# Optimization experiments

Hardware: AMD Instinct MI355X
Metric: run time of the kernel (lower is better)

The kernel has to match this reference:

```python
import jax, jax.numpy as jnp
import numpy as np

B, N_ATOMS = 8192, 64      # molecules, atoms per molecule
DIM, EXTRA, N_CLS = 70, 7, 11
N_FP = 10000               # fingerprint vocab


def setup_inputs() -> dict:
    key = jax.random.key(0)
    ks = jax.random.split(key, 9)
    atoms = jax.random.randint(ks[0], (B, N_ATOMS), 0, N_FP, dtype=jnp.int64 if jax.config.jax_enable_x64 else jnp.int32)
    adjacency = jax.random.uniform(ks[1], (B, N_ATOMS, N_ATOMS), dtype=jnp.float32)
    sel_desc = jax.random.normal(ks[2], (B, EXTRA), dtype=jnp.float32)
    embed_table = jax.random.normal(ks[3], (N_FP, DIM), dtype=jnp.float32)
    w1 = jax.random.normal(ks[4], (DIM, DIM), dtype=jnp.float32) * 0.05
    b1 = jax.random.normal(ks[5], (DIM,), dtype=jnp.float32) * 0.05
    w2 = jax.random.normal(ks[6], (DIM, DIM), dtype=jnp.float32) * 0.05
    b2 = jax.random.normal(ks[7], (DIM,), dtype=jnp.float32) * 0.05
    wp = jax.random.normal(ks[8], (DIM + EXTRA, N_CLS), dtype=jnp.float32) * 0.05
    bp = jnp.zeros((N_CLS,), dtype=jnp.float32)
    return {"atoms": atoms, "adjacency": adjacency, "sel_desc": sel_desc,
            "embed_table": embed_table, "w1": w1, "b1": b1,
            "w2": w2, "b2": b2, "wp": wp, "bp": bp}


def reference(atoms, adjacency, sel_desc, embed_table, w1, b1, w2, b2, wp, bp):
    # embed atoms: [B, n, dim]
    x = embed_table[atoms]
    # message-passing layers: relu(linear) then (block-diagonal == batched) adjacency matmul
    for w, b in ((w1, b1), (w2, b2)):
        h = jax.nn.relu(jnp.einsum('bnd,de->bne', x, w) + b)
        x = jnp.einsum('bnm,bmd->bnd', adjacency, h)
    # segment-sum pool over atoms per molecule (sum_axis)
    y = jnp.sum(x, axis=1)                       # [B, dim]
    y = jnp.concatenate([y, sel_desc], axis=1)   # [B, dim+extra]
    return jnp.einsum('bd,dc->bc', y, wp) + bp   # [B, 11]
```

## Files before the change

kernel.cpp:

```cpp
#include <hip/hip_runtime.h>
#include <hip/hip_bf16.h>

#define NFP    10000
#define DIM    70
#define GPAD   72
#define NATOMS 64
#define PGROWS 16

typedef short  short8  __attribute__((ext_vector_type(8)));
typedef float  floatx4 __attribute__((ext_vector_type(4)));

__device__ inline unsigned short f2bf(float f) {
  union { float f; unsigned u; } x; x.f = f;
  unsigned r = x.u + 0x7fffu + ((x.u >> 16) & 1u);
  return (unsigned short)(r >> 16);
}

__device__ inline ushort2 pk2bf(float a, float b) {
  __hip_bfloat162 h = __float22bfloat162_rn(make_float2(a, b));
  union { __hip_bfloat162 h; ushort2 u; } c; c.h = h; return c.u;
}

__global__ __launch_bounds__(256) void precompute_G(
    const float* __restrict__ emb, const float* __restrict__ w1,
    const float* __restrict__ b1,  const float* __restrict__ w2,
    unsigned short* __restrict__ G) {
  __shared__ float w1s[DIM * GPAD];
  __shared__ float w2s[DIM * GPAD];
  __shared__ float b1s[GPAD];
  __shared__ float embs[PGROWS * GPAD];
  __shared__ float e1s[PGROWS * GPAD];
  const int t = threadIdx.x;

  for (int i = t; i < DIM * GPAD; i += 256) {
    int r = i / GPAD, c = i % GPAD;
    float v1 = 0.f, v2 = 0.f;
    if (c < DIM) { v1 = w1[r * DIM + c]; v2 = w2[r * DIM + c]; }
    w1s[i] = v1; w2s[i] = v2;
  }
  if (t < GPAD) b1s[t] = (t < DIM) ? b1[t] : 0.f;
  const int row0 = blockIdx.x * PGROWS;
  for (int i = t; i < PGROWS * GPAD; i += 256) {
    int r = i / GPAD, c = i % GPAD;
    int vr = row0 + r;
    embs[i] = (vr < NFP && c < DIM) ? emb[vr * DIM + c] : 0.f;
  }
  __syncthreads();

  for (int task = t; task < PGROWS * 18; task += 256) {
    int r = task / 18, c4 = (task % 18) * 4;
    float4 acc = *(const float4*)&b1s[c4];
    for (int k = 0; k < DIM; k++) {
      float e = embs[r * GPAD + k];
      float4 w = *(const float4*)&w1s[k * GPAD + c4];
      acc.x = fmaf(e, w.x, acc.x); acc.y = fmaf(e, w.y, acc.y);
      acc.z = fmaf(e, w.z, acc.z); acc.w = fmaf(e, w.w, acc.w);
    }
    acc.x = fmaxf(acc.x, 0.f); acc.y = fmaxf(acc.y, 0.f);
    acc.z = fmaxf(acc.z, 0.f); acc.w = fmaxf(acc.w, 0.f);
    *(float4*)&e1s[r * GPAD + c4] = acc;
  }
  __syncthreads();

  for (int task = t; task < PGROWS * 18; task += 256) {
    int r = task / 18, c4 = (task % 18) * 4;
    int vr = row0 + r;
    if (vr >= NFP) continue;
    float ax = 0.f, ay = 0.f, az = 0.f, aw = 0.f;
    for (int k = 0; k < DIM; k++) {
      float e = e1s[r * GPAD + k];
      float4 w = *(const float4*)&w2s[k * GPAD + c4];
      ax = fmaf(e, w.x, ax); ay = fmaf(e, w.y, ay);
      az = fmaf(e, w.z, az); aw = fmaf(e, w.w, aw);
    }
    unsigned short* gp = G + vr * GPAD + c4;
    gp[0] = f2bf(ax); gp[1] = f2bf(ay); gp[2] = f2bf(az); gp[3] = f2bf(aw);
  }
}

__global__ __launch_bounds__(256) void mol_fused(
    const int* __restrict__ atoms, const float* __restrict__ adj,
    const float* __restrict__ sel, const float* __restrict__ b2,
    const float* __restrict__ wp,  const float* __restrict__ bp,
    const unsigned short* __restrict__ G, float* __restrict__ out) {
  __shared__ unsigned short adjs[64 * GPAD];
  __shared__ unsigned short gTs[80 * GPAD];
  __shared__ float cwave[4 * 64];
  __shared__ float b2p[80];
  __shared__ float yacc[4 * 80];
  __shared__ float yv[80];
  __shared__ int   satoms[64];

  const int b = blockIdx.x;
  const int t = threadIdx.x;
  const int w = t >> 6, lane = t & 63;
  const int q = lane >> 4, li = lane & 15;
  const int R = w * 16;

  if (t < 64) satoms[t] = atoms[b * 64 + t];
  if (t < 80) b2p[t] = (t < DIM) ? b2[t] : 0.f;
  __syncthreads();

  {
    const float* ap = adj + (size_t)b * 4096;
    const int mc = (t & 15) * 4;
    const int a  = t >> 4;
    float4 cs = make_float4(0.f, 0.f, 0.f, 0.f);
#pragma unroll
    for (int it = 0; it < 4; it++) {
      int n = a + 16 * it;
      float4 v = *(const float4*)(ap + n * 64 + mc);
      cs.x += v.x; cs.y += v.y; cs.z += v.z; cs.w += v.w;
      ushort2 lo = pk2bf(v.x, v.y);
      ushort2 hi = pk2bf(v.z, v.w);
      ushort4 u; u.x = lo.x; u.y = lo.y; u.z = hi.x; u.w = hi.y;
      *(ushort4*)&adjs[n * GPAD + mc] = u;
    }
#pragma unroll
    for (int s = 16; s <= 32; s <<= 1) {
      cs.x += __shfl_xor(cs.x, s); cs.y += __shfl_xor(cs.y, s);
      cs.z += __shfl_xor(cs.z, s); cs.w += __shfl_xor(cs.w, s);
    }
    if (((t >> 4) & 3) == 0) *(float4*)&cwave[w * 64 + mc] = cs;
  }

  {
    const int m = t & 63;
    const int row = satoms[m];
    const uint4* Gv = (const uint4*)G;
    for (int ch = w; ch < 9; ch += 4) {
      uint4 v = Gv[(unsigned)row * 9 + ch];
      unsigned short* gp = &gTs[(ch * 8) * GPAD + m];
      gp[0 * GPAD] = (unsigned short)(v.x & 0xffff);
      gp[1 * GPAD] = (unsigned short)(v.x >> 16);
      gp[2 * GPAD] = (unsigned short)(v.y & 0xffff);
      gp[3 * GPAD] = (unsigned short)(v.y >> 16);
      gp[4 * GPAD] = (unsigned short)(v.z & 0xffff);
      gp[5 * GPAD] = (unsigned short)(v.z >> 16);
      gp[6 * GPAD] = (unsigned short)(v.w & 0xffff);
      gp[7 * GPAD] = (unsigned short)(v.w >> 16);
    }
  }
  if (t < 72) {
    uint4 zz; zz.x = zz.y = zz.z = zz.w = 0u;
    *(uint4*)&gTs[72 * GPAD + t * 8] = zz;
  }
  __syncthreads();

  float cr[4];
#pragma unroll
  for (int r = 0; r < 4; r++) {
    int m = R + q * 4 + r;
    cr[r] = cwave[m] + cwave[64 + m] + cwave[128 + m] + cwave[192 + m];
  }

  short8 a0 = *(const short8*)&adjs[(R + li) * GPAD + q * 8];
  short8 a1 = *(const short8*)&adjs[(R + li) * GPAD + 32 + q * 8];
  floatx4 acc[5];
#pragma unroll
  for (int nt = 0; nt < 5; nt++) {
    floatx4 z = {0.f, 0.f, 0.f, 0.f};
    short8 b0 = *(const short8*)&gTs[(nt * 16 + li) * GPAD + q * 8];
    short8 b1 = *(const short8*)&gTs[(nt * 16 + li) * GPAD + 32 + q * 8];
    z = __builtin_amdgcn_mfma_f32_16x16x32_bf16(a0, b0, z, 0, 0, 0);
    z = __builtin_amdgcn_mfma_f32_16x16x32_bf16(a1, b1, z, 0, 0, 0);
    acc[nt] = z;
  }

  float ps[5];
#pragma unroll
  for (int nt = 0; nt < 5; nt++) {
    float bb = b2p[nt * 16 + li];
    float p = 0.f;
#pragma unroll
    for (int r = 0; r < 4; r++)
      p = fmaf(cr[r], fmaxf(acc[nt][r] + bb, 0.f), p);
    p += __shfl_xor(p, 16);
    p += __shfl_xor(p, 32);
    ps[nt] = p;
  }
  if (q == 0) {
#pragma unroll
    for (int nt = 0; nt < 5; nt++) yacc[w * 80 + nt * 16 + li] = ps[nt];
  }
  __syncthreads();

  if (t < 77) {
    float s;
    if (t < DIM) s = yacc[t] + yacc[80 + t] + yacc[160 + t] + yacc[240 + t];
    else         s = sel[(size_t)b * 7 + (t - DIM)];
    yv[t] = s;
  }
  __syncthreads();

  if (t < 11) {
    float s = bp[t];
#pragma unroll 11
    for (int d = 0; d < 77; d++) s = fmaf(yv[d], wp[d * 11 + t], s);
    out[(size_t)b * 11 + t] = s;
  }
}

extern "C" void kernel_launch(void* const* d_in, const int* in_sizes, int n_in,
                              void* d_out, int out_size, void* d_ws, size_t ws_size,
                              hipStream_t stream) {
  const int*   atoms = (const int*)d_in[0];
  const float* adj   = (const float*)d_in[1];
  const float* sel   = (const float*)d_in[2];
  const float* emb   = (const float*)d_in[3];
  const float* w1    = (const float*)d_in[4];
  const float* b1    = (const float*)d_in[5];
  const float* w2    = (const float*)d_in[6];
  const float* b2    = (const float*)d_in[7];
  const float* wp    = (const float*)d_in[8];
  const float* bp    = (const float*)d_in[9];

  const int B = in_sizes[0] / NATOMS;
  unsigned short* G = (unsigned short*)d_ws;

  precompute_G<<<(NFP + PGROWS - 1) / PGROWS, 256, 0, stream>>>(emb, w1, b1, w2, G);
  mol_fused<<<B, 256, 0, stream>>>(atoms, adj, sel, b2, wp, bp, G, (float*)d_out);
}
```

Measured before the change: 243.9 us.

## Hoist global loads, drop syncs, and parallelize final projection with wave shuffles

```diff
diff --git a/kernel.cpp b/kernel.cpp
--- a/kernel.cpp
+++ b/kernel.cpp
@@ -78,7 +78,7 @@
   }
 }
 
-__global__ __launch_bounds__(256) void mol_fused(
+__global__ __launch_bounds__(256, 7) void mol_fused(
     const int* __restrict__ atoms, const float* __restrict__ adj,
     const float* __restrict__ sel, const float* __restrict__ b2,
     const float* __restrict__ wp,  const float* __restrict__ bp,
@@ -86,72 +86,97 @@
   __shared__ unsigned short adjs[64 * GPAD];
   __shared__ unsigned short gTs[80 * GPAD];
   __shared__ float cwave[4 * 64];
-  __shared__ float b2p[80];
   __shared__ float yacc[4 * 80];
-  __shared__ float yv[80];
-  __shared__ int   satoms[64];
 
   const int b = blockIdx.x;
   const int t = threadIdx.x;
   const int w = t >> 6, lane = t & 63;
   const int q = lane >> 4, li = lane & 15;
   const int R = w * 16;
-
-  if (t < 64) satoms[t] = atoms[b * 64 + t];
-  if (t < 80) b2p[t] = (t < DIM) ? b2[t] : 0.f;
-  __syncthreads();
+  const int m = lane;
+
+  const int myAtom = atoms[b * 64 + m];
+  const float* ap = adj + (size_t)b * 4096;
+  const int mc = (t & 15) * 4;
+  const int a  = t >> 4;
+  float4 v0 = *(const float4*)(ap + (a     ) * 64 + mc);
+  float4 v1 = *(const float4*)(ap + (a + 16) * 64 + mc);
+  float4 v2 = *(const float4*)(ap + (a + 32) * 64 + mc);
+  float4 v3 = *(const float4*)(ap + (a + 48) * 64 + mc);
+  const uint4* Gv = (const uint4*)G;
+  uint4 g0 = Gv[(unsigned)myAtom * 9 + w];
+  uint4 g1 = Gv[(unsigned)myAtom * 9 + w + 4];
+  uint4 g2;
+  if (w == 0) g2 = Gv[(unsigned)myAtom * 9 + 8];
 
   {
-    const float* ap = adj + (size_t)b * 4096;
-    const int mc = (t & 15) * 4;
-    const int a  = t >> 4;
-    float4 cs = make_float4(0.f, 0.f, 0.f, 0.f);
-#pragma unroll
-    for (int it = 0; it < 4; it++) {
-      int n = a + 16 * it;
-      float4 v = *(const float4*)(ap + n * 64 + mc);
-      cs.x += v.x; cs.y += v.y; cs.z += v.z; cs.w += v.w;
-      ushort2 lo = pk2bf(v.x, v.y);
-      ushort2 hi = pk2bf(v.z, v.w);
-      ushort4 u; u.x = lo.x; u.y = lo.y; u.z = hi.x; u.w = hi.y;
-      *(ushort4*)&adjs[n * GPAD + mc] = u;
-    }
+    float4 cs;
+    cs.x = (v0.x + v1.x) + (v2.x + v3.x);
+    cs.y = (v0.y + v1.y) + (v2.y + v3.y);
+    cs.z = (v0.z + v1.z) + (v2.z + v3.z);
+    cs.w = (v0.w + v1.w) + (v2.w + v3.w);
 #pragma unroll
     for (int s = 16; s <= 32; s <<= 1) {
       cs.x += __shfl_xor(cs.x, s); cs.y += __shfl_xor(cs.y, s);
       cs.z += __shfl_xor(cs.z, s); cs.w += __shfl_xor(cs.w, s);
     }
     if (((t >> 4) & 3) == 0) *(float4*)&cwave[w * 64 + mc] = cs;
+
+    float4 vv[4] = {v0, v1, v2, v3};
+#pragma unroll
+    for (int it = 0; it < 4; it++) {
+      int n = a + 16 * it;
+      ushort2 lo = pk2bf(vv[it].x, vv[it].y);
+      ushort2 hi = pk2bf(vv[it].z, vv[it].w);
+      ushort4 u; u.x = lo.x; u.y = lo.y; u.z = hi.x; u.w = hi.y;
+      *(ushort4*)&adjs[n * GPAD + mc] = u;
+    }
   }
 
   {
-    const int m = t & 63;
-    const int row = satoms[m];
-    const uint4* Gv = (const uint4*)G;
-    for (int ch = w; ch < 9; ch += 4) {
-      uint4 v = Gv[(unsigned)row * 9 + ch];
-      unsigned short* gp = &gTs[(ch * 8) * GPAD + m];
-      gp[0 * GPAD] = (unsigned short)(v.x & 0xffff);
-      gp[1 * GPAD] = (unsigned short)(v.x >> 16);
-      gp[2 * GPAD] = (unsigned short)(v.y & 0xffff);
-      gp[3 * GPAD] = (unsigned short)(v.y >> 16);
-      gp[4 * GPAD] = (unsigned short)(v.z & 0xffff);
-      gp[5 * GPAD] = (unsigned short)(v.z >> 16);
-      gp[6 * GPAD] = (unsigned short)(v.w & 0xffff);
-      gp[7 * GPAD] = (unsigned short)(v.w >> 16);
-    }
-  }
-  if (t < 72) {
-    uint4 zz; zz.x = zz.y = zz.z = zz.w = 0u;
-    *(uint4*)&gTs[72 * GPAD + t * 8] = zz;
+    unsigned short* gp0 = &gTs[(w * 8) * GPAD + m];
+    gp0[0 * GPAD] = (unsigned short)(g0.x & 0xffff);
+    gp0[1 * GPAD] = (unsigned short)(g0.x >> 16);
+    gp0[2 * GPAD] = (unsigned short)(g0.y & 0xffff);
+    gp0[3 * GPAD] = (unsigned short)(g0.y >> 16);
+    gp0[4 * GPAD] = (unsigned short)(g0.z & 0xffff);
+    gp0[5 * GPAD] = (unsigned short)(g0.z >> 16);
+    gp0[6 * GPAD] = (unsigned short)(g0.w & 0xffff);
+    gp0[7 * GPAD] = (unsigned short)(g0.w >> 16);
+    unsigned short* gp1 = &gTs[((w + 4) * 8) * GPAD + m];
+    gp1[0 * GPAD] = (unsigned short)(g1.x & 0xffff);
+    gp1[1 * GPAD] = (unsigned short)(g1.x >> 16);
+    gp1[2 * GPAD] = (unsigned short)(g1.y & 0xffff);
+    gp1[3 * GPAD] = (unsigned short)(g1.y >> 16);
+    gp1[4 * GPAD] = (unsigned short)(g1.z & 0xffff);
+    gp1[5 * GPAD] = (unsigned short)(g1.z >> 16);
+    gp1[6 * GPAD] = (unsigned short)(g1.w & 0xffff);
+    gp1[7 * GPAD] = (unsigned short)(g1.w >> 16);
+    if (w == 0) {
+      unsigned short* gp2 = &gTs[64 * GPAD + m];
+      gp2[0 * GPAD] = (unsigned short)(g2.x & 0xffff);
+      gp2[1 * GPAD] = (unsigned short)(g2.x >> 16);
+      gp2[2 * GPAD] = (unsigned short)(g2.y & 0xffff);
+      gp2[3 * GPAD] = (unsigned short)(g2.y >> 16);
+      gp2[4 * GPAD] = (unsigned short)(g2.z & 0xffff);
+      gp2[5 * GPAD] = (unsigned short)(g2.z >> 16);
+      gp2[6 * GPAD] = (unsigned short)(g2.w & 0xffff);
+      gp2[7 * GPAD] = (unsigned short)(g2.w >> 16);
+    }
   }
   __syncthreads();
 
   float cr[4];
 #pragma unroll
   for (int r = 0; r < 4; r++) {
-    int m = R + q * 4 + r;
-    cr[r] = cwave[m] + cwave[64 + m] + cwave[128 + m] + cwave[192 + m];
+    int mm = R + q * 4 + r;
+    cr[r] = cwave[mm] + cwave[64 + mm] + cwave[128 + mm] + cwave[192 + mm];
+  }
+  float bbv[5];
+#pragma unroll
+  for (int nt = 0; nt < 5; nt++) {
+    int d = nt * 16 + li;
+    bbv[nt] = (d < DIM) ? b2[d] : 0.f;
   }
 
   short8 a0 = *(const short8*)&adjs[(R + li) * GPAD + q * 8];
@@ -167,37 +192,38 @@
     acc[nt] = z;
   }
 
-  float ps[5];
 #pragma unroll
   for (int nt = 0; nt < 5; nt++) {
-    float bb = b2p[nt * 16 + li];
+    float bb = bbv[nt];
     float p = 0.f;
 #pragma unroll
     for (int r = 0; r < 4; r++)
       p = fmaf(cr[r], fmaxf(acc[nt][r] + bb, 0.f), p);
     p += __shfl_xor(p, 16);
     p += __shfl_xor(p, 32);
-    ps[nt] = p;
-  }
-  if (q == 0) {
-#pragma unroll
-    for (int nt = 0; nt < 5; nt++) yacc[w * 80 + nt * 16 + li] = ps[nt];
-  }
-  __syncthreads();
-
-  if (t < 77) {
-    float s;
-    if (t < DIM) s = yacc[t] + yacc[80 + t] + yacc[160 + t] + yacc[240 + t];
-    else         s = sel[(size_t)b * 7 + (t - DIM)];
-    yv[t] = s;
-  }
-  __syncthreads();
-
-  if (t < 11) {
-    float s = bp[t];
-#pragma unroll 11
-    for (int d = 0; d < 77; d++) s = fmaf(yv[d], wp[d * 11 + t], s);
-    out[(size_t)b * 11 + t] = s;
+    if (q == 0) yacc[w * 80 + nt * 16 + li] = p;
+  }
+  __syncthreads();
+
+  if (w == 0) {
+    float val = yacc[lane] + yacc[80 + lane] + yacc[160 + lane] + yacc[240 + lane];
+    int d2 = 64 + lane;
+    float val2 = 0.f;
+    if (lane < 6)        val2 = yacc[d2] + yacc[80 + d2] + yacc[160 + d2] + yacc[240 + d2];
+    else if (lane < 13)  val2 = sel[(size_t)b * 7 + (d2 - DIM)];
+    float pc[11];
+#pragma unroll
+    for (int c = 0; c < 11; c++) pc[c] = val * wp[lane * 11 + c];
+    if (lane < 13) {
+#pragma unroll
+      for (int c = 0; c < 11; c++) pc[c] = fmaf(val2, wp[d2 * 11 + c], pc[c]);
+    }
+#pragma unroll
+    for (int s = 1; s <= 32; s <<= 1) {
+#pragma unroll
+      for (int c = 0; c < 11; c++) pc[c] += __shfl_xor(pc[c], s);
+    }
+    if (lane < 11) out[(size_t)b * 11 + lane] = pc[lane] + bp[lane];
   }
 }
 
```

New measurement: 233.3 us. -4.3%, faster.
